# Optimization experiments

Hardware: AMD Instinct MI355X
Metric: run time of the kernel (lower is better)

The kernel has to match this reference:

```python
import jax, jax.numpy as jnp
import numpy as np

EPS = 1e-8  # torch CosineSimilarity default eps


def setup_inputs() -> dict:
    key = jax.random.key(0)
    k1, k2 = jax.random.split(key)
    B, R, T, D = 128, 36, 128, 1024
    img_feats = jax.random.normal(k1, (B, R, D), dtype=jnp.float32)
    cap_feats = jax.random.normal(k2, (B, T, D), dtype=jnp.float32)
    cap_mask = jnp.ones((B, T), dtype=jnp.bool_)
    return {"img_feats": img_feats, "cap_feats": cap_feats, "cap_mask": cap_mask}


def reference(img_feats, cap_feats, cap_mask):
    # img_feats: [B, R, D], cap_feats: [B, T, D]; cap_mask unused (as in original forward)
    img = img_feats.reshape(-1, img_feats.shape[-2], img_feats.shape[-1])
    # cosine similarity between every region and every caption token
    dot = jnp.einsum('brd,btd->brt', img, cap_feats)            # [B, R, T]
    ni = jnp.linalg.norm(img, axis=-1)                          # [B, R]
    nc = jnp.linalg.norm(cap_feats, axis=-1)                    # [B, T]
    denom = jnp.maximum(ni[:, :, None] * nc[:, None, :], EPS)   # [B, R, T]
    scores = dot / denom
    # softmax over regions (dim=1 in torch)
    weights = jax.nn.softmax(scores, axis=1)                    # [B, R, T]
    # softmax-weighted pooling of image features per caption token
    return jnp.einsum('brt,brd->btd', weights, img)             # [B, T, D]
```

## Files before the change

kernel.cpp:

```cpp
#include <hip/hip_runtime.h>
#include <math.h>

#define NB 128
#define NR 36
#define NT 128
#define ND 1024
#define TTA 32
#define IST 1032
#define WST 64

typedef float    f32x4 __attribute__((ext_vector_type(4)));
typedef _Float16 f16x8 __attribute__((ext_vector_type(8)));
typedef _Float16 f16x4 __attribute__((ext_vector_type(4)));

__global__ __launch_bounds__(256, 2)
void scores_softmax(const float* __restrict__ img, const float* __restrict__ cap,
                    _Float16* __restrict__ w_ws) {
    __shared__ __align__(16) _Float16 img_c[NR][IST];
    __shared__ float sc_s[TTA][49];
    __shared__ float ni_s[NR];
    __shared__ float nc_s[TTA];

    const int tid  = threadIdx.x;
    const int phys = blockIdx.x;
    const int lb = (phys & 7) * 64 + (phys >> 3);
    const int b  = lb >> 2;
    const int t0 = (lb & 3) * TTA;

    const float* imgB = img + (size_t)b * NR * ND;
    const float* capB = cap + ((size_t)b * NT + t0) * ND;

    const int wv = tid >> 6, lane = tid & 63, ln = lane & 15, hi = lane >> 4;

    for (int i = tid; i < TTA * 49; i += 256) ((float*)sc_s)[i] = 0.f;
    if (tid < TTA) nc_s[tid] = 0.f;

    float nip[9];
    #pragma unroll
    for (int i = 0; i < 9; ++i) nip[i] = 0.f;
    #pragma unroll
    for (int j = 0; j < 36; ++j) {
        const int row = wv * 9 + (j >> 2);
        const int c4  = (j & 3) * 64 + lane;
        const float4 v = *(const float4*)(imgB + row * ND + c4 * 4);
        nip[j >> 2] = fmaf(v.x, v.x, fmaf(v.y, v.y, fmaf(v.z, v.z, fmaf(v.w, v.w, nip[j >> 2]))));
        f16x4 h; h[0] = (_Float16)v.x; h[1] = (_Float16)v.y;
                 h[2] = (_Float16)v.z; h[3] = (_Float16)v.w;
        *(f16x4*)(&img_c[row][c4 * 4]) = h;
    }
    #pragma unroll
    for (int jr = 0; jr < 9; ++jr) {
        float s = nip[jr];
        #pragma unroll
        for (int off = 32; off; off >>= 1) s += __shfl_xor(s, off, 64);
        if (lane == 0) ni_s[wv * 9 + jr] = sqrtf(s);
    }
    __syncthreads();

    const int th    = (wv & 1) * 16;
    const int kbase = (wv >> 1) * 512;

    const float* capR = capB + (size_t)(th + ln) * ND + kbase + hi * 8;
    const char*  bp0  = (const char*)&img_c[ln][0];
    const char*  bp1  = (const char*)&img_c[16 + ln][0];
    const char*  bp2  = (const char*)&img_c[32 + (ln < 4 ? ln : 3)][0];

    f32x4 acc0 = {0.f,0.f,0.f,0.f}, acc1 = acc0, acc2 = acc0;
    float ncp = 0.f;

    #pragma unroll
    for (int step = 0; step < 16; ++step) {
        const float4 u0 = *(const float4*)(capR + step * 32);
        const float4 u1 = *(const float4*)(capR + step * 32 + 4);
        ncp = fmaf(u0.x,u0.x, fmaf(u0.y,u0.y, fmaf(u0.z,u0.z, fmaf(u0.w,u0.w, ncp))));
        ncp = fmaf(u1.x,u1.x, fmaf(u1.y,u1.y, fmaf(u1.z,u1.z, fmaf(u1.w,u1.w, ncp))));
        f16x8 a;
        a[0] = (_Float16)u0.x; a[1] = (_Float16)u0.y; a[2] = (_Float16)u0.z; a[3] = (_Float16)u0.w;
        a[4] = (_Float16)u1.x; a[5] = (_Float16)u1.y; a[6] = (_Float16)u1.z; a[7] = (_Float16)u1.w;
        const int koff2 = (kbase + step * 32 + hi * 8) * 2;
        const f16x8 b0 = *(const f16x8*)(bp0 + koff2);
        const f16x8 b1 = *(const f16x8*)(bp1 + koff2);
        const f16x8 b2 = *(const f16x8*)(bp2 + koff2);
        acc0 = __builtin_amdgcn_mfma_f32_16x16x32_f16(a, b0, acc0, 0, 0, 0);
        acc1 = __builtin_amdgcn_mfma_f32_16x16x32_f16(a, b1, acc1, 0, 0, 0);
        acc2 = __builtin_amdgcn_mfma_f32_16x16x32_f16(a, b2, acc2, 0, 0, 0);
    }

    #pragma unroll
    for (int j = 0; j < 4; ++j) {
        atomicAdd(&sc_s[th + hi*4 + j][ln],      acc0[j]);
        atomicAdd(&sc_s[th + hi*4 + j][16 + ln], acc1[j]);
        atomicAdd(&sc_s[th + hi*4 + j][32 + ln], acc2[j]);
    }
    {
        float s = ncp;
        s += __shfl_xor(s, 16, 64);
        s += __shfl_xor(s, 32, 64);
        if (lane < 16) atomicAdd(&nc_s[th + ln], s);
    }
    __syncthreads();

    if (tid < TTA) {
        const float nct = sqrtf(nc_s[tid]);
        float v[NR];
        float m = -1e30f;
        #pragma unroll
        for (int r = 0; r < NR; ++r) {
            const float d = fmaxf(ni_s[r] * nct, 1e-8f);
            v[r] = sc_s[tid][r] / d;
            m = fmaxf(m, v[r]);
        }
        float sum = 0.f;
        #pragma unroll
        for (int r = 0; r < NR; ++r) { v[r] = __expf(v[r] - m); sum += v[r]; }
        const float inv = 1.f / sum;
        _Float16* wO = w_ws + (size_t)(b * NT + t0 + tid) * WST;
        #pragma unroll
        for (int q = 0; q < 8; ++q) {
            f16x8 h;
            #pragma unroll
            for (int j = 0; j < 8; ++j) {
                const int r = q * 8 + j;
                h[j] = (r < NR) ? (_Float16)(v[r] * inv) : (_Float16)0.f;
            }
            *(f16x8*)(wO + q * 8) = h;
        }
    }
}

__global__ __launch_bounds__(256, 4)
void pool_mfma(const float* __restrict__ img, const _Float16* __restrict__ w_ws,
               float* __restrict__ out) {
    const int tid  = threadIdx.x;
    const int phys = blockIdx.x;
    const int lb = (phys & 7) * 256 + (phys >> 3);
    const int b  = lb >> 4;
    const int tq = (lb >> 2) & 3;
    const int dq = lb & 3;
    const int t0 = tq * 32;

    const int wv = tid >> 6, lane = tid & 63, ln = lane & 15, hi = lane >> 4;
    const int dw = dq * 256 + wv * 64;

    const float*    imgB = img  + (size_t)b * NR * ND;
    const _Float16* wB   = w_ws + (size_t)(b * NT + t0) * WST;
    float*          outB = out  + ((size_t)(b * NT + t0)) * ND;

    f16x8 afr[2][2];
    #pragma unroll
    for (int mfr = 0; mfr < 2; ++mfr)
        #pragma unroll
        for (int kk = 0; kk < 2; ++kk)
            afr[mfr][kk] = *(const f16x8*)(wB + (mfr * 16 + ln) * WST + kk * 32 + hi * 8);

    f32x4 acc[2][4];
    #pragma unroll
    for (int mfr = 0; mfr < 2; ++mfr)
        #pragma unroll
        for (int nf = 0; nf < 4; ++nf)
            acc[mfr][nf] = (f32x4){0.f, 0.f, 0.f, 0.f};

    #pragma unroll
    for (int nf = 0; nf < 4; ++nf) {
        const int dcol = dw + nf * 16 + ln;
        #pragma unroll
        for (int kk = 0; kk < 2; ++kk) {
            f16x8 bfr;
            #pragma unroll
            for (int j = 0; j < 8; ++j) {
                int r = kk * 32 + hi * 8 + j;
                if (r >= NR) r = NR - 1;
                bfr[j] = (_Float16)imgB[r * ND + dcol];
            }
            #pragma unroll
            for (int mfr = 0; mfr < 2; ++mfr)
                acc[mfr][nf] = __builtin_amdgcn_mfma_f32_16x16x32_f16(afr[mfr][kk], bfr, acc[mfr][nf], 0, 0, 0);
        }
    }

    #pragma unroll
    for (int mfr = 0; mfr < 2; ++mfr)
        #pragma unroll
        for (int nf = 0; nf < 4; ++nf)
            #pragma unroll
            for (int j = 0; j < 4; ++j)
                outB[(size_t)(mfr * 16 + hi * 4 + j) * ND + dw + nf * 16 + ln] = acc[mfr][nf][j];
}

extern "C" void kernel_launch(void* const* d_in, const int* in_sizes, int n_in,
                              void* d_out, int out_size, void* d_ws, size_t ws_size,
                              hipStream_t stream) {
    const float* img = (const float*)d_in[0];
    const float* cap = (const float*)d_in[1];
    float* out = (float*)d_out;
    _Float16* w_ws = (_Float16*)d_ws;

    scores_softmax<<<NB * 4, 256, 0, stream>>>(img, cap, w_ws);
    pool_mfma<<<NB * 16, 256, 0, stream>>>(img, w_ws, out);
}
```

Measured before the change: 44.42 us.

## Double-buffer image chunks via async global-to-LDS loads in scores kernel

The scores kernel no longer stages the whole image tile as fp16 in LDS before the GEMM. It now streams 256-column fp32 chunks into a double-buffered LDS array with global_load_lds, so loading the next chunk overlaps computing the current one. K is also re-split across waves per chunk, and the norms are taken from the LDS copy. The aim is to hide the serialized upfront image load, at the cost of more barriers, larger fp32 LDS reads, and fp16 conversions inside the MFMA loop.

```diff
diff --git a/kernel.cpp b/kernel.cpp
--- a/kernel.cpp
+++ b/kernel.cpp
@@ -6,17 +6,38 @@
 #define NT 128
 #define ND 1024
 #define TTA 32
-#define IST 1032
+#define BST 258
 #define WST 64
 
 typedef float    f32x4 __attribute__((ext_vector_type(4)));
 typedef _Float16 f16x8 __attribute__((ext_vector_type(8)));
-typedef _Float16 f16x4 __attribute__((ext_vector_type(4)));
+
+__device__ __forceinline__ f16x8 cvt8(const float4 a, const float4 b) {
+    f16x8 h;
+    h[0] = (_Float16)a.x; h[1] = (_Float16)a.y; h[2] = (_Float16)a.z; h[3] = (_Float16)a.w;
+    h[4] = (_Float16)b.x; h[5] = (_Float16)b.y; h[6] = (_Float16)b.z; h[7] = (_Float16)b.w;
+    return h;
+}
+__device__ __forceinline__ f16x8 cvt8v(const f32x4 a, const f32x4 b) {
+    f16x8 h;
+    h[0] = (_Float16)a[0]; h[1] = (_Float16)a[1]; h[2] = (_Float16)a[2]; h[3] = (_Float16)a[3];
+    h[4] = (_Float16)b[0]; h[5] = (_Float16)b[1]; h[6] = (_Float16)b[2]; h[7] = (_Float16)b[3];
+    return h;
+}
+__device__ __forceinline__ float sq8(const float4 a, const float4 b, float s) {
+    s = fmaf(a.x,a.x, fmaf(a.y,a.y, fmaf(a.z,a.z, fmaf(a.w,a.w, s))));
+    return fmaf(b.x,b.x, fmaf(b.y,b.y, fmaf(b.z,b.z, fmaf(b.w,b.w, s))));
+}
+__device__ __forceinline__ void gload_lds16(const float* g, float* l) {
+    __builtin_amdgcn_global_load_lds(
+        (const __attribute__((address_space(1))) void*)g,
+        (__attribute__((address_space(3))) void*)l, 16, 0, 0);
+}
 
 __global__ __launch_bounds__(256, 2)
 void scores_softmax(const float* __restrict__ img, const float* __restrict__ cap,
                     _Float16* __restrict__ w_ws) {
-    __shared__ __align__(16) _Float16 img_c[NR][IST];
+    __shared__ __align__(16) float buf[2][NR][BST];
     __shared__ float sc_s[TTA][49];
     __shared__ float ni_s[NR];
     __shared__ float nc_s[TTA];
@@ -31,72 +52,89 @@
     const float* capB = cap + ((size_t)b * NT + t0) * ND;
 
     const int wv = tid >> 6, lane = tid & 63, ln = lane & 15, hi = lane >> 4;
+    const int tg = wv & 1;
+    const int kq = wv >> 1;
 
     for (int i = tid; i < TTA * 49; i += 256) ((float*)sc_s)[i] = 0.f;
     if (tid < TTA) nc_s[tid] = 0.f;
 
-    float nip[9];
-    #pragma unroll
-    for (int i = 0; i < 9; ++i) nip[i] = 0.f;
-    #pragma unroll
-    for (int j = 0; j < 36; ++j) {
-        const int row = wv * 9 + (j >> 2);
-        const int c4  = (j & 3) * 64 + lane;
-        const float4 v = *(const float4*)(imgB + row * ND + c4 * 4);
-        nip[j >> 2] = fmaf(v.x, v.x, fmaf(v.y, v.y, fmaf(v.z, v.z, fmaf(v.w, v.w, nip[j >> 2]))));
-        f16x4 h; h[0] = (_Float16)v.x; h[1] = (_Float16)v.y;
-                 h[2] = (_Float16)v.z; h[3] = (_Float16)v.w;
-        *(f16x4*)(&img_c[row][c4 * 4]) = h;
-    }
-    #pragma unroll
-    for (int jr = 0; jr < 9; ++jr) {
-        float s = nip[jr];
+    #pragma unroll
+    for (int j = 0; j < 9; ++j) {
+        const int row = wv * 9 + j;
+        gload_lds16(imgB + (size_t)row * ND + lane * 4, &buf[0][row][0]);
+    }
+
+    const float* capR = capB + (size_t)(tg * 16 + ln) * ND + kq * 128 + hi * 8;
+
+    float nip[9] = {0.f,0.f,0.f,0.f,0.f,0.f,0.f,0.f,0.f};
+    float ncp = 0.f;
+    f32x4 acc0 = {0.f,0.f,0.f,0.f}, acc1 = acc0, acc2 = acc0;
+
+    for (int c = 0; c < 4; ++c) {
+        __syncthreads();
+        const float* bc = &buf[c & 1][0][0];
+
+        float4 pc0 = *(const float4*)(capR + c*256);
+        float4 pc1 = *(const float4*)(capR + c*256 + 4);
+        float4 pc2 = *(const float4*)(capR + c*256 + 32);
+        float4 pc3 = *(const float4*)(capR + c*256 + 36);
+        float4 pc4 = *(const float4*)(capR + c*256 + 64);
+        float4 pc5 = *(const float4*)(capR + c*256 + 68);
+        float4 pc6 = *(const float4*)(capR + c*256 + 96);
+        float4 pc7 = *(const float4*)(capR + c*256 + 100);
+
+        if (c < 3) {
+            #pragma unroll
+            for (int j = 0; j < 9; ++j) {
+                const int row = wv * 9 + j;
+                gload_lds16(imgB + (size_t)row * ND + (c + 1) * 256 + lane * 4,
+                            &buf[(c + 1) & 1][row][0]);
+            }
+        }
+
+        #pragma unroll
+        for (int j = 0; j < 9; ++j) {
+            const f32x4 v = *(const f32x4*)(bc + (size_t)(wv * 9 + j) * BST + lane * 4);
+            nip[j] = fmaf(v[0],v[0], fmaf(v[1],v[1], fmaf(v[2],v[2], fmaf(v[3],v[3], nip[j]))));
+        }
+
+        const float* r0 = bc + (size_t)ln * BST;
+        const float* r1 = bc + (size_t)(16 + ln) * BST;
+        const float* r2 = bc + (size_t)(32 + (ln < 4 ? ln : 3)) * BST;
+        #pragma unroll
+        for (int s = 0; s < 4; ++s) {
+            const float4 ua = (s==0)?pc0:(s==1)?pc2:(s==2)?pc4:pc6;
+            const float4 ub = (s==0)?pc1:(s==1)?pc3:(s==2)?pc5:pc7;
+            ncp = sq8(ua, ub, ncp);
+            const f16x8 a = cvt8(ua, ub);
+            const int ko = kq * 128 + s * 32 + hi * 8;
+            const f16x8 b0 = cvt8v(*(const f32x4*)(r0 + ko), *(const f32x4*)(r0 + ko + 4));
+            const f16x8 b1 = cvt8v(*(const f32x4*)(r1 + ko), *(const f32x4*)(r1 + ko + 4));
+            const f16x8 b2 = cvt8v(*(const f32x4*)(r2 + ko), *(const f32x4*)(r2 + ko + 4));
+            acc0 = __builtin_amdgcn_mfma_f32_16x16x32_f16(a, b0, acc0, 0, 0, 0);
+            acc1 = __builtin_amdgcn_mfma_f32_16x16x32_f16(a, b1, acc1, 0, 0, 0);
+            acc2 = __builtin_amdgcn_mfma_f32_16x16x32_f16(a, b2, acc2, 0, 0, 0);
+        }
+    }
+
+    #pragma unroll
+    for (int j = 0; j < 4; ++j) {
+        atomicAdd(&sc_s[tg * 16 + hi*4 + j][ln],      acc0[j]);
+        atomicAdd(&sc_s[tg * 16 + hi*4 + j][16 + ln], acc1[j]);
+        atomicAdd(&sc_s[tg * 16 + hi*4 + j][32 + ln], acc2[j]);
+    }
+    #pragma unroll
+    for (int j = 0; j < 9; ++j) {
+        float s = nip[j];
         #pragma unroll
         for (int off = 32; off; off >>= 1) s += __shfl_xor(s, off, 64);
-        if (lane == 0) ni_s[wv * 9 + jr] = sqrtf(s);
-    }
-    __syncthreads();
-
-    const int th    = (wv & 1) * 16;
-    const int kbase = (wv >> 1) * 512;
-
-    const float* capR = capB + (size_t)(th + ln) * ND + kbase + hi * 8;
-    const char*  bp0  = (const char*)&img_c[ln][0];
-    const char*  bp1  = (const char*)&img_c[16 + ln][0];
-    const char*  bp2  = (const char*)&img_c[32 + (ln < 4 ? ln : 3)][0];
-
-    f32x4 acc0 = {0.f,0.f,0.f,0.f}, acc1 = acc0, acc2 = acc0;
-    float ncp = 0.f;
-
-    #pragma unroll
-    for (int step = 0; step < 16; ++step) {
-        const float4 u0 = *(const float4*)(capR + step * 32);
-        const float4 u1 = *(const float4*)(capR + step * 32 + 4);
-        ncp = fmaf(u0.x,u0.x, fmaf(u0.y,u0.y, fmaf(u0.z,u0.z, fmaf(u0.w,u0.w, ncp))));
-        ncp = fmaf(u1.x,u1.x, fmaf(u1.y,u1.y, fmaf(u1.z,u1.z, fmaf(u1.w,u1.w, ncp))));
-        f16x8 a;
-        a[0] = (_Float16)u0.x; a[1] = (_Float16)u0.y; a[2] = (_Float16)u0.z; a[3] = (_Float16)u0.w;
-        a[4] = (_Float16)u1.x; a[5] = (_Float16)u1.y; a[6] = (_Float16)u1.z; a[7] = (_Float16)u1.w;
-        const int koff2 = (kbase + step * 32 + hi * 8) * 2;
-        const f16x8 b0 = *(const f16x8*)(bp0 + koff2);
-        const f16x8 b1 = *(const f16x8*)(bp1 + koff2);
-        const f16x8 b2 = *(const f16x8*)(bp2 + koff2);
-        acc0 = __builtin_amdgcn_mfma_f32_16x16x32_f16(a, b0, acc0, 0, 0, 0);
-        acc1 = __builtin_amdgcn_mfma_f32_16x16x32_f16(a, b1, acc1, 0, 0, 0);
-        acc2 = __builtin_amdgcn_mfma_f32_16x16x32_f16(a, b2, acc2, 0, 0, 0);
-    }
-
-    #pragma unroll
-    for (int j = 0; j < 4; ++j) {
-        atomicAdd(&sc_s[th + hi*4 + j][ln],      acc0[j]);
-        atomicAdd(&sc_s[th + hi*4 + j][16 + ln], acc1[j]);
-        atomicAdd(&sc_s[th + hi*4 + j][32 + ln], acc2[j]);
+        if (lane == 0) ni_s[wv * 9 + j] = sqrtf(s);
     }
     {
         float s = ncp;
         s += __shfl_xor(s, 16, 64);
         s += __shfl_xor(s, 32, 64);
-        if (lane < 16) atomicAdd(&nc_s[th + ln], s);
+        if (lane < 16) atomicAdd(&nc_s[tg * 16 + ln], s);
     }
     __syncthreads();
 
```

After: 64.93 us. +46.2%, slower.
